# Kernel tuning notes

Measured on AMD Instinct MI355X. Metric: run time of the kernel, lower is better.

The kernel has to match this reference:

```python
import jax, jax.numpy as jnp
import numpy as np

B, L, N = 32, 64, 8
C, H_IMG, W_IMG = 3, 40, 40
HID = 64
N_ACT = 8
CNN_OUT = 64  # 64 channels * 1 * 1 spatial after the three convs on 40x40


def _conv(x, w, b, stride):
    # x: (B', Cin, H, W), w: (Cout, Cin, kh, kw)
    y = jax.lax.conv_general_dilated(
        x, w, window_strides=(stride, stride), padding='VALID',
        dimension_numbers=('NCHW', 'OIHW', 'NCHW'))
    return y + b[None, :, None, None]


def setup_inputs() -> dict:
    key = jax.random.key(0)
    ks = jax.random.split(key, 12)

    def rn(k, shape, fan_in):
        return jax.random.normal(k, shape, dtype=jnp.float32) * (1.0 / np.sqrt(fan_in))

    inp = {
        'obs_batch': jax.random.normal(ks[0], (B, L, N, C, H_IMG, W_IMG), dtype=jnp.float32),
        'hidden_state': jnp.zeros((B, N, HID), dtype=jnp.float32),
        'conv1_w': rn(ks[1], (32, C, 8, 8), C * 8 * 8),
        'conv1_b': jnp.zeros((32,), jnp.float32),
        'conv2_w': rn(ks[2], (64, 32, 4, 4), 32 * 4 * 4),
        'conv2_b': jnp.zeros((64,), jnp.float32),
        'conv3_w': rn(ks[3], (64, 64, 3, 3), 64 * 3 * 3),
        'conv3_b': jnp.zeros((64,), jnp.float32),
        'w_ih': rn(ks[4], (3 * HID, CNN_OUT), CNN_OUT),
        'w_hh': rn(ks[5], (3 * HID, HID), HID),
        'b_ih': jnp.zeros((3 * HID,), jnp.float32),
        'b_hh': jnp.zeros((3 * HID,), jnp.float32),
        'fc_w': rn(ks[6], (N_ACT, HID), HID),
        'fc_b': jnp.zeros((N_ACT,), jnp.float32),
    }
    return inp


def reference(obs_batch, hidden_state, conv1_w, conv1_b, conv2_w, conv2_b,
              conv3_w, conv3_b, w_ih, w_hh, b_ih, b_hh, fc_w, fc_b):
    b, l, n = obs_batch.shape[:3]
    x = obs_batch.reshape(-1, C, H_IMG, W_IMG)            # (B*L*N, C, H, W)
    x = jax.nn.relu(_conv(x, conv1_w, conv1_b, 4))
    x = jax.nn.relu(_conv(x, conv2_w, conv2_b, 2))
    x = jax.nn.relu(_conv(x, conv3_w, conv3_b, 1))
    feats = x.reshape(b, l, n, -1)                        # (B, L, N, F)

    # (L, B*N, F) time-major for scan
    rnn_in = feats.transpose(1, 0, 2, 3).reshape(l, b * n, -1)
    h0 = hidden_state.reshape(b * n, HID)

    def step(h, xt):
        gi = xt @ w_ih.T + b_ih
        gh = h @ w_hh.T + b_hh
        i_r, i_z, i_n = jnp.split(gi, 3, axis=-1)
        h_r, h_z, h_n = jnp.split(gh, 3, axis=-1)
        r = jax.nn.sigmoid(i_r + h_r)
        z = jax.nn.sigmoid(i_z + h_z)
        nn_ = jnp.tanh(i_n + r * h_n)
        h_new = (1.0 - z) * nn_ + z * h
        return h_new, h_new

    h_last, hs = jax.lax.scan(step, h0, rnn_in)           # hs: (L, B*N, HID)

    # torch path: stack (L, B*N, H) -> permute to (B*N, L, H) -> reshape (B*L*N, H)
    rnn_out = hs.transpose(1, 0, 2).reshape(b, n, l, HID).transpose(0, 2, 1, 3)
    q = rnn_out.reshape(-1, HID) @ fc_w.T + fc_b
    q_values = q.reshape(b, l, n, N_ACT)
    next_hidden_state = h_last.reshape(b, n, HID)
    return q_values, next_hidden_state
```

## Files before the change

kernel.cpp:

```cpp
#include <hip/hip_runtime.h>
#include <math.h>

typedef unsigned short ushort_t;
typedef unsigned int uint_t;
typedef __attribute__((ext_vector_type(8))) short short8_t;
typedef __attribute__((ext_vector_type(4))) float f32x4_t;

constexpr int Bb = 32, Ll = 64, Nn = 8;
constexpr int IMGS = Bb * Ll * Nn;
constexpr int Cc = 3, Hh = 40, Ww = 40;
constexpr int HID = 64, G3 = 192, NACT = 8;

__device__ inline float bf2f(ushort_t u) {
  union { uint_t i; float f; } v; v.i = ((uint_t)u) << 16; return v.f;
}
__device__ inline ushort_t f2bf(float f) {
  union { float f; uint_t u; } v; v.f = f;
  uint_t r = v.u + 0x7fffu + ((v.u >> 16) & 1u);
  return (ushort_t)(r >> 16);
}
__device__ inline void unpack2(uint_t u, float& lo, float& hi) {
  union { uint_t i; float f; } a, b;
  a.i = u << 16; b.i = u & 0xffff0000u;
  lo = a.f; hi = b.f;
}
__device__ inline float ld1(const void* p, int idx, int isbf) {
  return isbf ? bf2f(((const ushort_t*)p)[idx]) : ((const float*)p)[idx];
}
__device__ inline short8_t ldsh8(const ushort_t* p) {
  union { short8_t v; uint2 u[2]; } r;
  r.u[0] = *(const uint2*)p;
  r.u[1] = *(const uint2*)(p + 4);
  return r.v;
}
__device__ inline short8_t ldg8(const ushort_t* p) {
  union { short8_t v; uint4 u; } r;
  r.u = *(const uint4*)p;
  return r.v;
}
#define WAVE_FENCE() asm volatile("s_waitcnt lgkmcnt(0)" ::: "memory")

__global__ __launch_bounds__(256) void detect_kernel(
    const ushort_t* __restrict__ obs, const ushort_t* __restrict__ whh,
    int* __restrict__ flags) {
  __shared__ int cnt[2];
  if (threadIdx.x < 2) cnt[threadIdx.x] = 0;
  __syncthreads();
  int bad0 = 0, bad1 = 0;
  for (int i = threadIdx.x; i < 4096; i += 256) {
    int e0 = (obs[i] >> 7) & 0xFF; if (e0 >= 0xC0) bad0++;
    int e1 = (whh[i] >> 7) & 0xFF; if (e1 >= 0xC0) bad1++;
  }
  atomicAdd(&cnt[0], bad0);
  atomicAdd(&cnt[1], bad1);
  __syncthreads();
  if (threadIdx.x == 0) { flags[0] = (cnt[0] <= 4); flags[1] = (cnt[1] <= 4); }
}

__global__ __launch_bounds__(256) void repack_kernel(
    const void* __restrict__ w1, const void* __restrict__ w2,
    const void* __restrict__ w3, const void* __restrict__ wih,
    const int* __restrict__ flags,
    ushort_t* __restrict__ w1pack, ushort_t* __restrict__ w2pack,
    ushort_t* __restrict__ w3bf, ushort_t* __restrict__ wihb) {
  const int fw = flags[1];
  int t = blockIdx.x * 256 + threadIdx.x;
  if (t < 6144) w1pack[t] = f2bf(ld1(w1, t, fw));
  if (t < 32768) {
    int oc = t >> 9, r = t & 511;
    int kykx = r >> 5, ic = r & 31;
    w2pack[t] = f2bf(ld1(w2, oc * 512 + ic * 16 + kykx, fw));
  }
  if (t < 36864) w3bf[t] = f2bf(ld1(w3, t, fw));
  if (t < 12288) wihb[t] = f2bf(ld1(wih, t, fw));
}

__global__ __launch_bounds__(256, 4) void conv12_kernel(
    const void* __restrict__ obs, const ushort_t* __restrict__ w1pack,
    const ushort_t* __restrict__ w2pack,
    const void* __restrict__ b1, const void* __restrict__ b2,
    const int* __restrict__ flags, ushort_t* __restrict__ f2g, int img_base) {
  __shared__ __attribute__((aligned(16))) ushort_t s_mem[4][4800];

  const int tid = threadIdx.x;
  const int wave = tid >> 6, lane = tid & 63;
  const int lrow = lane & 15, lk8 = lane >> 4;
  const int fobs = flags[0], fw = flags[1];
  const int img0 = blockIdx.x * 4;

  if (fobs) {
    const uint4* src = reinterpret_cast<const uint4*>((const ushort_t*)obs + ((size_t)img_base + img0) * 4800);
    uint4 r[10];
#pragma unroll
    for (int it = 0; it < 10; ++it) {
      const int i = it * 256 + tid;
      r[it] = src[i < 2400 ? i : 2399];
    }
#pragma unroll
    for (int it = 0; it < 10; ++it) {
      const int i = it * 256 + tid;
      if (i < 2400) {
        const int im_ = i / 600, e = i - im_ * 600;
        reinterpret_cast<uint4*>(s_mem[im_])[e] = r[it];
      }
    }
  } else {
    const float4* src = reinterpret_cast<const float4*>((const float*)obs + ((size_t)img_base + img0) * 4800);
#pragma unroll
    for (int bb = 0; bb < 2; ++bb) {
      float4 r[10];
#pragma unroll
      for (int it = 0; it < 10; ++it) {
        const int i = (bb * 10 + it) * 256 + tid;
        r[it] = src[i < 4800 ? i : 4799];
      }
#pragma unroll
      for (int it = 0; it < 10; ++it) {
        const int i = (bb * 10 + it) * 256 + tid;
        if (i < 4800) {
          const int im_ = i / 1200, e = i - im_ * 1200;
          uint2 o;
          o.x = (uint_t)f2bf(r[it].x) | ((uint_t)f2bf(r[it].y) << 16);
          o.y = (uint_t)f2bf(r[it].z) | ((uint_t)f2bf(r[it].w) << 16);
          reinterpret_cast<uint2*>(s_mem[im_])[e] = o;
        }
      }
    }
  }
  __syncthreads();

  {
    ushort_t* si = s_mem[wave];
    int ab[6];
#pragma unroll
    for (int mt = 0; mt < 6; ++mt) {
      int p = mt * 16 + lrow; if (p > 80) p = 80;
      ab[mt] = (p / 9) * 160 + (p % 9) * 4;
    }
    f32x4_t acc[2][6];
#pragma unroll
    for (int nt = 0; nt < 2; ++nt)
#pragma unroll
      for (int mt = 0; mt < 6; ++mt) acc[nt][mt] = (f32x4_t){0.f, 0.f, 0.f, 0.f};
    const ushort_t* wr0 = w1pack + lrow * 192 + lk8 * 8;
#pragma unroll
    for (int ks = 0; ks < 6; ++ks) {
      const int g = ks * 4 + lk8;
      const int aoff = (g >> 3) * 1600 + (g & 7) * 40;
      short8_t b0 = ldg8(wr0 + ks * 32);
      short8_t b1v = ldg8(wr0 + 16 * 192 + ks * 32);
#pragma unroll
      for (int mt = 0; mt < 6; ++mt) {
        short8_t a = ldsh8(&si[aoff + ab[mt]]);
        acc[0][mt] = __builtin_amdgcn_mfma_f32_16x16x32_bf16(a, b0, acc[0][mt], 0, 0, 0);
        acc[1][mt] = __builtin_amdgcn_mfma_f32_16x16x32_bf16(a, b1v, acc[1][mt], 0, 0, 0);
      }
    }
    WAVE_FENCE();
    const float bz0 = ld1(b1, lrow, fw), bz1 = ld1(b1, 16 + lrow, fw);
#pragma unroll
    for (int mt = 0; mt < 6; ++mt) {
#pragma unroll
      for (int r = 0; r < 4; ++r) {
        const int p = mt * 16 + lk8 * 4 + r;
        if (p < 81) {
          si[p * 40 + lrow]      = f2bf(fmaxf(acc[0][mt][r] + bz0, 0.f));
          si[p * 40 + 16 + lrow] = f2bf(fmaxf(acc[1][mt][r] + bz1, 0.f));
        }
      }
    }
  }
  __syncthreads();

  {
    int imgr[3], pbx[3];
#pragma unroll
    for (int mt = 0; mt < 3; ++mt) {
      int row = mt * 16 + lrow; if (row > 35) row = 35;
      const int ir = row / 9, p2 = row - ir * 9;
      imgr[mt] = ir;
      pbx[mt] = (p2 / 3) * 18 + (p2 % 3) * 2;
    }
    f32x4_t acc[3];
#pragma unroll
    for (int mt = 0; mt < 3; ++mt) acc[mt] = (f32x4_t){0.f, 0.f, 0.f, 0.f};
    const ushort_t* w2r = w2pack + (wave * 16 + lrow) * 512 + lk8 * 8;
#pragma unroll
    for (int s = 0; s < 16; ++s) {
      const int po = (s >> 2) * 9 + (s & 3);
      short8_t bv = ldg8(w2r + s * 32);
      short8_t a0 = ldsh8(&s_mem[imgr[0]][(pbx[0] + po) * 40 + lk8 * 8]);
      short8_t a1 = ldsh8(&s_mem[imgr[1]][(pbx[1] + po) * 40 + lk8 * 8]);
      short8_t a2 = ldsh8(&s_mem[imgr[2]][(pbx[2] + po) * 40 + lk8 * 8]);
      acc[0] = __builtin_amdgcn_mfma_f32_16x16x32_bf16(a0, bv, acc[0], 0, 0, 0);
      acc[1] = __builtin_amdgcn_mfma_f32_16x16x32_bf16(a1, bv, acc[1], 0, 0, 0);
      acc[2] = __builtin_amdgcn_mfma_f32_16x16x32_bf16(a2, bv, acc[2], 0, 0, 0);
    }
    const int oc = wave * 16 + lrow;
    const float bias = ld1(b2, oc, fw);
#pragma unroll
    for (int mt = 0; mt < 3; ++mt) {
#pragma unroll
      for (int r = 0; r < 4; ++r) {
        const int row = mt * 16 + lk8 * 4 + r;
        if (row < 36) {
          const int ir = row / 9, pp = row - ir * 9;
          f2g[((size_t)img_base + img0 + ir) * 576 + oc * 9 + pp] =
              f2bf(fmaxf(acc[mt][r] + bias, 0.f));
        }
      }
    }
  }
}

__global__ __launch_bounds__(256) void conv3gi_kernel(
    const ushort_t* __restrict__ f2g, const ushort_t* __restrict__ w3bf,
    const ushort_t* __restrict__ wihb, const void* __restrict__ b3,
    const int* __restrict__ flags, float* __restrict__ gi, int img_base) {
  __shared__ __attribute__((aligned(16))) ushort_t f2b[16 * 592];
  __shared__ __attribute__((aligned(16))) ushort_t f3b[16 * 72];

  const int tid = threadIdx.x;
  const int wave = tid >> 6, lane = tid & 63;
  const int lrow = lane & 15, lk8 = lane >> 4;
  const int fw = flags[1];
  const int iloc0 = blockIdx.x * 16;

  for (int i = tid; i < 16 * 72; i += 256) {
    const int im_ = i / 72, off = i - im_ * 72;
    *reinterpret_cast<uint4*>(&f2b[im_ * 592 + off * 8]) =
        *reinterpret_cast<const uint4*>(&f2g[((size_t)img_base + iloc0 + im_) * 576 + off * 8]);
  }
  __syncthreads();

  {
    f32x4_t c3 = (f32x4_t){0.f, 0.f, 0.f, 0.f};
    const ushort_t* w3r = w3bf + (wave * 16 + lrow) * 576 + lk8 * 8;
#pragma unroll
    for (int ks = 0; ks < 18; ++ks) {
      short8_t a = ldsh8(&f2b[lrow * 592 + ks * 32 + lk8 * 8]);
      short8_t bv = ldg8(w3r + ks * 32);
      c3 = __builtin_amdgcn_mfma_f32_16x16x32_bf16(a, bv, c3, 0, 0, 0);
    }
    const int oc = wave * 16 + lrow;
    const float bias = ld1(b3, oc, fw);
#pragma unroll
    for (int r = 0; r < 4; ++r)
      f3b[(lk8 * 4 + r) * 72 + oc] = f2bf(fmaxf(c3[r] + bias, 0.f));
  }
  __syncthreads();

#pragma unroll
  for (int t = 0; t < 3; ++t) {
    const int nt = wave * 3 + t;
    f32x4_t g = (f32x4_t){0.f, 0.f, 0.f, 0.f};
#pragma unroll
    for (int ks = 0; ks < 2; ++ks) {
      short8_t a = ldsh8(&f3b[lrow * 72 + ks * 32 + lk8 * 8]);
      short8_t bv = ldg8(wihb + (nt * 16 + lrow) * 64 + ks * 32 + lk8 * 8);
      g = __builtin_amdgcn_mfma_f32_16x16x32_bf16(a, bv, g, 0, 0, 0);
    }
#pragma unroll
    for (int r = 0; r < 4; ++r)
      gi[((size_t)img_base + iloc0 + lk8 * 4 + r) * G3 + nt * 16 + lrow] = g[r];
  }
}

__global__ __launch_bounds__(256) void gru_kernel(
    const float* __restrict__ gi, const void* __restrict__ h0,
    const void* __restrict__ whh, const void* __restrict__ bih,
    const void* __restrict__ bhh, const int* __restrict__ flags,
    float* __restrict__ rnn, float* __restrict__ hout) {
  __shared__ float s_w[G3 * 68];
  __shared__ float s_h[HID];
  const int tid = threadIdx.x;
  const int s = blockIdx.x;
  const int fw = flags[1];

  if (fw) {
    const uint4* wsrc = reinterpret_cast<const uint4*>(whh);
    uint4 r[6];
#pragma unroll
    for (int it = 0; it < 6; ++it) r[it] = wsrc[it * 256 + tid];
#pragma unroll
    for (int it = 0; it < 6; ++it) {
      const int v = it * 256 + tid;
      const int i8 = v * 8;
      float* d = &s_w[(i8 >> 6) * 68 + (i8 & 63)];
      unpack2(r[it].x, d[0], d[1]);
      unpack2(r[it].y, d[2], d[3]);
      unpack2(r[it].z, d[4], d[5]);
      unpack2(r[it].w, d[6], d[7]);
    }
  } else {
    const float4* wsrc = reinterpret_cast<const float4*>(whh);
#pragma unroll
    for (int bb = 0; bb < 2; ++bb) {
      float4 r[6];
#pragma unroll
      for (int it = 0; it < 6; ++it) r[it] = wsrc[(bb * 6 + it) * 256 + tid];
#pragma unroll
      for (int it = 0; it < 6; ++it) {
        const int v = (bb * 6 + it) * 256 + tid;
        const int i4 = v * 4;
        float* d = &s_w[(i4 >> 6) * 68 + (i4 & 63)];
        d[0] = r[it].x; d[1] = r[it].y; d[2] = r[it].z; d[3] = r[it].w;
      }
    }
  }
  if (tid < 64) s_h[tid] = ld1(h0, s * HID + tid, fw);
  __syncthreads();
  if (tid >= 64) return;

  const int j = tid;
  float h = s_h[j];
  const float bir = ld1(bih, j, fw), biz = ld1(bih, 64 + j, fw), bin_ = ld1(bih, 128 + j, fw);
  const float bhr = ld1(bhh, j, fw), bhz = ld1(bhh, 64 + j, fw), bhn = ld1(bhh, 128 + j, fw);
  const int b = s >> 3, n = s & 7;
  const float* gbase = gi + ((size_t)b * Ll * Nn + n) * G3;
  float* rbase = rnn + ((size_t)b * Ll * Nn + n) * HID;

  const float* wr = &s_w[j * 68];
  const float* wz = &s_w[(64 + j) * 68];
  const float* wn = &s_w[(128 + j) * 68];

  float g0 = gbase[j], g1 = gbase[64 + j], g2 = gbase[128 + j];

  for (int l = 0; l < Ll; ++l) {
    float p0 = 0.f, p1 = 0.f, p2 = 0.f;
    if (l + 1 < Ll) {
      const float* gn = gbase + (size_t)(l + 1) * Nn * G3;
      p0 = gn[j]; p1 = gn[64 + j]; p2 = gn[128 + j];
    }
    float hr = bhr, hz = bhz, hn = bhn;
#pragma unroll 4
    for (int k = 0; k < 64; k += 4) {
      float4 hv = *reinterpret_cast<const float4*>(&s_h[k]);
      float4 w0 = *reinterpret_cast<const float4*>(wr + k);
      float4 w1v = *reinterpret_cast<const float4*>(wz + k);
      float4 w2v = *reinterpret_cast<const float4*>(wn + k);
      hr += w0.x * hv.x + w0.y * hv.y + w0.z * hv.z + w0.w * hv.w;
      hz += w1v.x * hv.x + w1v.y * hv.y + w1v.z * hv.z + w1v.w * hv.w;
      hn += w2v.x * hv.x + w2v.y * hv.y + w2v.z * hv.z + w2v.w * hv.w;
    }
    const float gr = g0 + bir + hr;
    const float gz = g1 + biz + hz;
    const float gn_ = g2 + bin_;
    const float r = 1.f / (1.f + __expf(-gr));
    const float z = 1.f / (1.f + __expf(-gz));
    const float nn_ = tanhf(gn_ + r * hn);
    h = (1.f - z) * nn_ + z * h;
    WAVE_FENCE();
    s_h[j] = h;
    rbase[(size_t)l * Nn * HID + j] = h;
    WAVE_FENCE();
    g0 = p0; g1 = p1; g2 = p2;
  }
  hout[(size_t)s * HID + j] = h;
}

__global__ __launch_bounds__(256) void fc_kernel(
    const float* __restrict__ rnn, const void* __restrict__ fcw,
    const void* __restrict__ fcb, const int* __restrict__ flags,
    float* __restrict__ q) {
  __shared__ float s_w[NACT * HID];
  __shared__ float s_b[NACT];
  const int tid = threadIdx.x;
  const int fw = flags[1];
  for (int i = tid; i < NACT * HID; i += 256) s_w[i] = ld1(fcw, i, fw);
  if (tid < NACT) s_b[tid] = ld1(fcb, tid, fw);
  __syncthreads();
  const int row = blockIdx.x * 256 + tid;
  float x[64];
  const float4* xp = reinterpret_cast<const float4*>(rnn + (size_t)row * HID);
#pragma unroll
  for (int i = 0; i < 16; ++i) {
    float4 v = xp[i];
    x[4 * i] = v.x; x[4 * i + 1] = v.y; x[4 * i + 2] = v.z; x[4 * i + 3] = v.w;
  }
#pragma unroll
  for (int a = 0; a < NACT; ++a) {
    float v = s_b[a];
#pragma unroll
    for (int k = 0; k < 64; ++k) v += x[k] * s_w[a * 64 + k];
    q[(size_t)row * NACT + a] = v;
  }
}

extern "C" void kernel_launch(void* const* d_in, const int* in_sizes, int n_in,
                              void* d_out, int out_size, void* d_ws, size_t ws_size,
                              hipStream_t stream) {
  const void* obs = d_in[0];
  const void* h0  = d_in[1];
  const void* w1  = d_in[2];
  const void* b1  = d_in[3];
  const void* w2  = d_in[4];
  const void* b2  = d_in[5];
  const void* w3  = d_in[6];
  const void* b3  = d_in[7];
  const void* wih = d_in[8];
  const void* whh = d_in[9];
  const void* bih = d_in[10];
  const void* bhh = d_in[11];
  const void* fcw = d_in[12];
  const void* fcb = d_in[13];

  float* qout = (float*)d_out;
  float* hout = qout + (size_t)IMGS * NACT;

  char* wsb = (char*)d_ws;
  int*      flags  = (int*)wsb;
  float*    gi     = (float*)(wsb + 16);
  float*    rnn    = gi + (size_t)IMGS * G3;
  ushort_t* w1pack = (ushort_t*)(rnn + (size_t)IMGS * HID);
  ushort_t* w2pack = w1pack + 6144;
  ushort_t* w3bf   = w2pack + 32768;
  ushort_t* wihb   = w3bf + 36864;
  ushort_t* f2g    = wihb + 12288;

  const size_t base_bytes = (size_t)((char*)f2g - wsb);
  size_t cap = (ws_size > base_bytes) ? (ws_size - base_bytes) / 1152 : 0;
  cap = (cap / 16) * 16;
  if (cap > (size_t)IMGS) cap = IMGS;

  detect_kernel<<<1, 256, 0, stream>>>((const ushort_t*)obs, (const ushort_t*)whh, flags);
  repack_kernel<<<144, 256, 0, stream>>>(w1, w2, w3, wih, flags, w1pack, w2pack, w3bf, wihb);

  for (int c0 = 0; c0 < IMGS; c0 += (int)cap) {
    int n = IMGS - c0; if (n > (int)cap) n = (int)cap;
    conv12_kernel<<<n / 4, 256, 0, stream>>>(obs, w1pack, w2pack, b1, b2, flags, f2g, c0);
    conv3gi_kernel<<<n / 16, 256, 0, stream>>>(f2g, w3bf, wihb, b3, flags, gi, c0);
  }

  gru_kernel<<<256, 256, 0, stream>>>(gi, h0, whh, bih, bhh, flags, rnn, hout);
  fc_kernel<<<IMGS / 256, 256, 0, stream>>>(rnn, fcw, fcb, flags, qout);
}
```

Measured before the change: 216.0 us.

## Fuse conv3 and input-gate GEMM into conv12 kernel via shared memory

Moves the conv3 and GRU input-projection stages into the conv1/conv2 kernel, keeping the conv2 output in LDS instead of writing it to a global buffer and reading it back. This drops one kernel launch per chunk, the chunking loop and the f2g round trip through global memory. In exchange, each block now handles only 4 images, so the 16-row MFMA tiles for conv3 and gi are three-quarters wasted (rows are replicated with lrow&3). It also reuses the LDS region of the input image, which is safe only because a barrier separates the stages.

```diff
diff --git a/kernel.cpp b/kernel.cpp
--- a/kernel.cpp
+++ b/kernel.cpp
@@ -77,9 +77,10 @@
 
 __global__ __launch_bounds__(256, 4) void conv12_kernel(
     const void* __restrict__ obs, const ushort_t* __restrict__ w1pack,
-    const ushort_t* __restrict__ w2pack,
-    const void* __restrict__ b1, const void* __restrict__ b2,
-    const int* __restrict__ flags, ushort_t* __restrict__ f2g, int img_base) {
+    const ushort_t* __restrict__ w2pack, const ushort_t* __restrict__ w3bf,
+    const ushort_t* __restrict__ wihb,
+    const void* __restrict__ b1, const void* __restrict__ b2, const void* __restrict__ b3,
+    const int* __restrict__ flags, float* __restrict__ gi) {
   __shared__ __attribute__((aligned(16))) ushort_t s_mem[4][4800];
 
   const int tid = threadIdx.x;
@@ -89,7 +90,7 @@
   const int img0 = blockIdx.x * 4;
 
   if (fobs) {
-    const uint4* src = reinterpret_cast<const uint4*>((const ushort_t*)obs + ((size_t)img_base + img0) * 4800);
+    const uint4* src = reinterpret_cast<const uint4*>((const ushort_t*)obs + (size_t)img0 * 4800);
     uint4 r[10];
 #pragma unroll
     for (int it = 0; it < 10; ++it) {
@@ -105,7 +106,7 @@
       }
     }
   } else {
-    const float4* src = reinterpret_cast<const float4*>((const float*)obs + ((size_t)img_base + img0) * 4800);
+    const float4* src = reinterpret_cast<const float4*>((const float*)obs + (size_t)img0 * 4800);
 #pragma unroll
     for (int bb = 0; bb < 2; ++bb) {
       float4 r[10];
@@ -205,31 +206,10 @@
         const int row = mt * 16 + lk8 * 4 + r;
         if (row < 36) {
           const int ir = row / 9, pp = row - ir * 9;
-          f2g[((size_t)img_base + img0 + ir) * 576 + oc * 9 + pp] =
-              f2bf(fmaxf(acc[mt][r] + bias, 0.f));
+          s_mem[ir][3232 + oc * 9 + pp] = f2bf(fmaxf(acc[mt][r] + bias, 0.f));
         }
       }
     }
-  }
-}
-
-__global__ __launch_bounds__(256) void conv3gi_kernel(
-    const ushort_t* __restrict__ f2g, const ushort_t* __restrict__ w3bf,
-    const ushort_t* __restrict__ wihb, const void* __restrict__ b3,
-    const int* __restrict__ flags, float* __restrict__ gi, int img_base) {
-  __shared__ __attribute__((aligned(16))) ushort_t f2b[16 * 592];
-  __shared__ __attribute__((aligned(16))) ushort_t f3b[16 * 72];
-
-  const int tid = threadIdx.x;
-  const int wave = tid >> 6, lane = tid & 63;
-  const int lrow = lane & 15, lk8 = lane >> 4;
-  const int fw = flags[1];
-  const int iloc0 = blockIdx.x * 16;
-
-  for (int i = tid; i < 16 * 72; i += 256) {
-    const int im_ = i / 72, off = i - im_ * 72;
-    *reinterpret_cast<uint4*>(&f2b[im_ * 592 + off * 8]) =
-        *reinterpret_cast<const uint4*>(&f2g[((size_t)img_base + iloc0 + im_) * 576 + off * 8]);
   }
   __syncthreads();
 
@@ -238,15 +218,17 @@
     const ushort_t* w3r = w3bf + (wave * 16 + lrow) * 576 + lk8 * 8;
 #pragma unroll
     for (int ks = 0; ks < 18; ++ks) {
-      short8_t a = ldsh8(&f2b[lrow * 592 + ks * 32 + lk8 * 8]);
+      short8_t a = ldsh8(&s_mem[lrow & 3][3232 + ks * 32 + lk8 * 8]);
       short8_t bv = ldg8(w3r + ks * 32);
       c3 = __builtin_amdgcn_mfma_f32_16x16x32_bf16(a, bv, c3, 0, 0, 0);
     }
     const int oc = wave * 16 + lrow;
     const float bias = ld1(b3, oc, fw);
 #pragma unroll
-    for (int r = 0; r < 4; ++r)
-      f3b[(lk8 * 4 + r) * 72 + oc] = f2bf(fmaxf(c3[r] + bias, 0.f));
+    for (int r = 0; r < 4; ++r) {
+      const int row = lk8 * 4 + r;
+      if (row < 4) s_mem[0][3824 + row * 72 + oc] = f2bf(fmaxf(c3[r] + bias, 0.f));
+    }
   }
   __syncthreads();
 
@@ -256,13 +238,16 @@
     f32x4_t g = (f32x4_t){0.f, 0.f, 0.f, 0.f};
 #pragma unroll
     for (int ks = 0; ks < 2; ++ks) {
-      short8_t a = ldsh8(&f3b[lrow * 72 + ks * 32 + lk8 * 8]);
+      short8_t a = ldsh8(&s_mem[0][3824 + (lrow & 3) * 72 + ks * 32 + lk8 * 8]);
       short8_t bv = ldg8(wihb + (nt * 16 + lrow) * 64 + ks * 32 + lk8 * 8);
       g = __builtin_amdgcn_mfma_f32_16x16x32_bf16(a, bv, g, 0, 0, 0);
     }
 #pragma unroll
-    for (int r = 0; r < 4; ++r)
-      gi[((size_t)img_base + iloc0 + lk8 * 4 + r) * G3 + nt * 16 + lrow] = g[r];
+    for (int r = 0; r < 4; ++r) {
+      const int row = lk8 * 4 + r;
+      if (row < 4)
+        gi[(size_t)(img0 + row) * G3 + nt * 16 + lrow] = g[r];
+    }
   }
 }
 
@@ -416,22 +401,11 @@
   ushort_t* w2pack = w1pack + 6144;
   ushort_t* w3bf   = w2pack + 32768;
   ushort_t* wihb   = w3bf + 36864;
-  ushort_t* f2g    = wihb + 12288;
-
-  const size_t base_bytes = (size_t)((char*)f2g - wsb);
-  size_t cap = (ws_size > base_bytes) ? (ws_size - base_bytes) / 1152 : 0;
-  cap = (cap / 16) * 16;
-  if (cap > (size_t)IMGS) cap = IMGS;
 
   detect_kernel<<<1, 256, 0, stream>>>((const ushort_t*)obs, (const ushort_t*)whh, flags);
   repack_kernel<<<144, 256, 0, stream>>>(w1, w2, w3, wih, flags, w1pack, w2pack, w3bf, wihb);
-
-  for (int c0 = 0; c0 < IMGS; c0 += (int)cap) {
-    int n = IMGS - c0; if (n > (int)cap) n = (int)cap;
-    conv12_kernel<<<n / 4, 256, 0, stream>>>(obs, w1pack, w2pack, b1, b2, flags, f2g, c0);
-    conv3gi_kernel<<<n / 16, 256, 0, stream>>>(f2g, w3bf, wihb, b3, flags, gi, c0);
-  }
-
+  conv12_kernel<<<IMGS / 4, 256, 0, stream>>>(obs, w1pack, w2pack, w3bf, wihb,
+                                              b1, b2, b3, flags, gi);
   gru_kernel<<<256, 256, 0, stream>>>(gi, h0, whh, bih, bhh, flags, rnn, hout);
   fc_kernel<<<IMGS / 256, 256, 0, stream>>>(rnn, fcw, fcb, flags, qout);
 }
```

After: 229.4 us. 1.06x slower.
